# Kernel optimization log

Measured on AMD Instinct MI355X. Metric: run time of the kernel, lower is better.

Reference implementation:

```python
import jax, jax.numpy as jnp
import numpy as np

N_BINS = 15  # matches ECELoss(n_bins=15)


def setup_inputs() -> dict:
    key = jax.random.key(0)
    k1, k2 = jax.random.split(key)
    B, C = 2_097_152, 16
    logits = jax.random.normal(k1, (B, C), dtype=jnp.float32) * 2.0
    # binary multi-label targets, stored as float (forward casts to float anyway)
    targets = (jax.random.uniform(k2, (B, C)) < 0.5).astype(jnp.float32)
    return {"logits": logits, "targets": targets}


def reference(logits, targets):
    """Vectorized ECE: single bucketize + segment-sum pass replacing the
    per-class/per-bin Python loops. Same math: for each non-empty (class, bin)
    cell, accumulate |mean_conf - mean_acc| * (cell_count / B), then divide by
    the number of non-empty cells."""
    B, C = logits.shape
    probs = jax.nn.sigmoid(logits)  # [B, C]
    boundaries = jnp.linspace(0.0, 1.0, N_BINS + 1)
    # bin b satisfies boundaries[b] <= p < boundaries[b+1]  (>= start, < end)
    bin_idx = jnp.searchsorted(boundaries, probs, side="right") - 1  # [B, C]
    valid = (bin_idx >= 0) & (bin_idx < N_BINS)  # p == 1.0 falls in no bin
    seg = jnp.where(valid, jnp.arange(C)[None, :] * N_BINS + bin_idx, C * N_BINS)
    seg = seg.reshape(-1)
    num_seg = C * N_BINS + 1  # last segment = dumping ground for invalid
    ones = jnp.ones((B * C,), dtype=probs.dtype)
    cnt = jax.ops.segment_sum(ones, seg, num_segments=num_seg)[:-1]           # [C*n_bins]
    sum_p = jax.ops.segment_sum(probs.reshape(-1), seg, num_segments=num_seg)[:-1]
    sum_t = jax.ops.segment_sum(targets.reshape(-1), seg, num_segments=num_seg)[:-1]
    nonempty = cnt > 0
    safe = jnp.where(nonempty, cnt, 1.0)
    # |avg_confidence - accuracy| * mask.mean()  per non-empty cell
    term = jnp.abs(sum_p / safe - sum_t / safe) * (cnt / B)
    total = jnp.sum(jnp.where(nonempty, term, 0.0))
    count = jnp.sum(nonempty)
    return jnp.where(count > 0, total / count, jnp.zeros((), probs.dtype))
```

## Files before the change

### kernel.cpp

```cpp
#include <hip/hip_runtime.h>
#include <math.h>

#define NC 16
#define NBINS 15
#define NCELL (NC * NBINS)
#define GRID 2048
#define VITERS 16
#define BROWS 2097152.0
#define MAXREP 8

typedef float floatx4 __attribute__((ext_vector_type(4)));

template <int CTRL>
__device__ __forceinline__ unsigned int dpp_add(unsigned int v) {
    return v + (unsigned int)__builtin_amdgcn_update_dpp(0, (int)v, CTRL, 0xF, 0xF, true);
}

__device__ __forceinline__ float4 ldnt(const float4* p) {
    floatx4 v = __builtin_nontemporal_load((const floatx4*)p);
    return make_float4(v.x, v.y, v.z, v.w);
}

__global__ void __launch_bounds__(256, 4)
ece_partial(const float4* __restrict__ logits,
            const float4* __restrict__ targets,
            float* __restrict__ ws, int nrep) {
    __shared__ unsigned int h[64 * 60];

    const float LOG2E = 1.4426950408889634f;
    const int tid = blockIdx.x * 256 + threadIdx.x;
    const int S   = GRID * 256;

    unsigned int acc[4][NBINS];
#pragma unroll
    for (int j = 0; j < 4; ++j)
#pragma unroll
        for (int b = 0; b < NBINS; ++b) acc[j][b] = 0u;

    for (int k = 0; k < VITERS; k += 2) {
        int i0 = tid + k * S, i1 = i0 + S;
        float4 la[2], ta[2];
        la[0] = ldnt(&logits[i0]);
        la[1] = ldnt(&logits[i1]);
        ta[0] = targets[i0];
        ta[1] = targets[i1];
#pragma unroll
        for (int m = 0; m < 2; ++m) {
            float xs[4]  = {la[m].x, la[m].y, la[m].z, la[m].w};
            float tvs[4] = {ta[m].x, ta[m].y, ta[m].z, ta[m].w};
            int bs[4];
            unsigned int us[4];
#pragma unroll
            for (int j = 0; j < 4; ++j) {
                float e = __builtin_amdgcn_exp2f(-xs[j] * LOG2E);
                float p = __builtin_amdgcn_rcpf(1.0f + e);
                bs[j] = (int)(p * 15.0f);
                us[j] = (unsigned int)(fmaf(tvs[j], 262144.0f,
                                            fmaf(p, 1024.0f, 0.5f))) + (1u << 25);
            }
#pragma unroll
            for (int j = 0; j < 4; ++j)
#pragma unroll
                for (int b = 0; b < NBINS; ++b)
                    acc[j][b] += (bs[j] == b) ? us[j] : 0u;
        }
    }

#pragma unroll
    for (int j = 0; j < 4; ++j)
#pragma unroll
        for (int b = 0; b < NBINS; ++b) {
            unsigned int v = acc[j][b];
            v = dpp_add<0x114>(v);
            v = dpp_add<0x118>(v);
            acc[j][b] = v;
        }

    const int lane = threadIdx.x & 63;
    const int w    = threadIdx.x >> 6;
    const int r    = lane >> 4;
    const int q    = lane & 3;
    if ((lane & 15) >= 12) {
        unsigned int* dst = &h[((w * 4 + r) * 4 + q) * 60];
#pragma unroll
        for (int j = 0; j < 4; ++j)
#pragma unroll
            for (int b = 0; b < NBINS; ++b) dst[j * NBINS + b] = acc[j][b];
    }
    __syncthreads();

    const int t = threadIdx.x;
    if (t < NCELL) {
        const int bb = t >> 4;
        const int c  = t & 15;
        const int qq = c >> 2, jj = c & 3;
        unsigned int cnt = 0, tsum = 0, psum = 0;
#pragma unroll
        for (int m = 0; m < 16; ++m) {
            unsigned int v = h[(m * 4 + qq) * 60 + jj * NBINS + bb];
            cnt  += v >> 25;
            tsum += (v >> 18) & 127u;
            psum += v & 0x3FFFFu;
        }
        float* rp = ws + (blockIdx.x & (nrep - 1)) * (3 * NCELL);
        atomicAdd(&rp[t],             (float)cnt);
        atomicAdd(&rp[NCELL + t],     (float)psum * (1.0f / 1024.0f));
        atomicAdd(&rp[2 * NCELL + t], (float)tsum);
    }
}

__global__ void __launch_bounds__(256) ece_final(const float* __restrict__ ws,
                                                 float* __restrict__ out, int nrep) {
    __shared__ double s_term[256];
    __shared__ int s_ne[256];
    int i = threadIdx.x;
    double term = 0.0;
    int ne = 0;
    if (i < NCELL) {
        float cnt = 0.0f, sp = 0.0f, st = 0.0f;
        for (int rep = 0; rep < nrep; ++rep) {
            const float* r = ws + rep * (3 * NCELL);
            cnt += r[i];
            sp  += r[NCELL + i];
            st  += r[2 * NCELL + i];
        }
        if (cnt > 0.0f) {
            ne = 1;
            term = fabs((double)sp / (double)cnt - (double)st / (double)cnt) *
                   ((double)cnt / BROWS);
        }
    }
    s_term[i] = term;
    s_ne[i] = ne;
    __syncthreads();
    for (int off = 128; off > 0; off >>= 1) {
        if (i < off) {
            s_term[i] += s_term[i + off];
            s_ne[i]   += s_ne[i + off];
        }
        __syncthreads();
    }
    if (i == 0) out[0] = (s_ne[0] > 0) ? (float)(s_term[0] / (double)s_ne[0]) : 0.0f;
}

extern "C" void kernel_launch(void* const* d_in, const int* in_sizes, int n_in,
                              void* d_out, int out_size, void* d_ws, size_t ws_size,
                              hipStream_t stream) {
    const float4* logits  = (const float4*)d_in[0];
    const float4* targets = (const float4*)d_in[1];
    float* ws  = (float*)d_ws;
    float* out = (float*)d_out;

    int nrep = MAXREP;
    while (nrep > 1 && (size_t)(nrep * 3 * NCELL * sizeof(float)) > ws_size) nrep >>= 1;

    (void)hipMemsetAsync(ws, 0, nrep * 3 * NCELL * sizeof(float), stream);
    ece_partial<<<GRID, 256, 0, stream>>>(logits, targets, ws, nrep);
    ece_final<<<1, 256, 0, stream>>>(ws, out, nrep);
}
```

Baseline: 269.1 us.

## Replace register select-accumulate histogram with per-thread LDS atomic bins

Each thread now adds its packed value into a private column of a 64x256 LDS histogram with an atomic add, instead of running 15 compare-and-select adds per element in registers. Loads are batched four at a time instead of two. The aim is to cut the ALU work of the one-hot accumulation. The cost is 64 KB of LDS per block, which lowers occupancy (launch bounds go from 4 to 2), plus LDS atomic latency and extra barriers.

Result: no change. 270.3 us (+0.4%).

```diff
diff --git a/kernel.cpp b/kernel.cpp
--- a/kernel.cpp
+++ b/kernel.cpp
@@ -21,50 +21,53 @@
     return make_float4(v.x, v.y, v.z, v.w);
 }
 
-__global__ void __launch_bounds__(256, 4)
+__global__ void __launch_bounds__(256, 2)
 ece_partial(const float4* __restrict__ logits,
             const float4* __restrict__ targets,
             float* __restrict__ ws, int nrep) {
-    __shared__ unsigned int h[64 * 60];
+    __shared__ unsigned int h1[64 * 256];
 
     const float LOG2E = 1.4426950408889634f;
     const int tid = blockIdx.x * 256 + threadIdx.x;
     const int S   = GRID * 256;
+    const int col = threadIdx.x;
 
-    unsigned int acc[4][NBINS];
 #pragma unroll
-    for (int j = 0; j < 4; ++j)
+    for (int r = 0; r < 64; ++r) h1[r * 256 + col] = 0u;
+    __syncthreads();
+
+    for (int k = 0; k < VITERS; k += 4) {
+        float4 lv[4], tv[4];
 #pragma unroll
-        for (int b = 0; b < NBINS; ++b) acc[j][b] = 0u;
-
-    for (int k = 0; k < VITERS; k += 2) {
-        int i0 = tid + k * S, i1 = i0 + S;
-        float4 la[2], ta[2];
-        la[0] = ldnt(&logits[i0]);
-        la[1] = ldnt(&logits[i1]);
-        ta[0] = targets[i0];
-        ta[1] = targets[i1];
+        for (int m = 0; m < 4; ++m) {
+            int i = tid + (k + m) * S;
+            lv[m] = ldnt(&logits[i]);
+            tv[m] = targets[i];
+        }
 #pragma unroll
-        for (int m = 0; m < 2; ++m) {
-            float xs[4]  = {la[m].x, la[m].y, la[m].z, la[m].w};
-            float tvs[4] = {ta[m].x, ta[m].y, ta[m].z, ta[m].w};
-            int bs[4];
-            unsigned int us[4];
+        for (int m = 0; m < 4; ++m) {
+            float xs[4]  = {lv[m].x, lv[m].y, lv[m].z, lv[m].w};
+            float tvs[4] = {tv[m].x, tv[m].y, tv[m].z, tv[m].w};
 #pragma unroll
             for (int j = 0; j < 4; ++j) {
                 float e = __builtin_amdgcn_exp2f(-xs[j] * LOG2E);
                 float p = __builtin_amdgcn_rcpf(1.0f + e);
-                bs[j] = (int)(p * 15.0f);
-                us[j] = (unsigned int)(fmaf(tvs[j], 262144.0f,
-                                            fmaf(p, 1024.0f, 0.5f))) + (1u << 25);
+                int b = ((int)(p * 15.0f)) & 15;
+                unsigned int u = (unsigned int)(fmaf(tvs[j], 262144.0f,
+                                                     fmaf(p, 1024.0f, 0.5f))) +
+                                 (1u << 25);
+                atomicAdd(&h1[(b * 4 + j) * 256 + col], u);
             }
-#pragma unroll
-            for (int j = 0; j < 4; ++j)
-#pragma unroll
-                for (int b = 0; b < NBINS; ++b)
-                    acc[j][b] += (bs[j] == b) ? us[j] : 0u;
         }
     }
+    __syncthreads();
+
+    unsigned int acc[4][NBINS];
+#pragma unroll
+    for (int b = 0; b < NBINS; ++b)
+#pragma unroll
+        for (int j = 0; j < 4; ++j) acc[j][b] = h1[(b * 4 + j) * 256 + col];
+    __syncthreads();
 
 #pragma unroll
     for (int j = 0; j < 4; ++j)
@@ -81,7 +84,7 @@
     const int r    = lane >> 4;
     const int q    = lane & 3;
     if ((lane & 15) >= 12) {
-        unsigned int* dst = &h[((w * 4 + r) * 4 + q) * 60];
+        unsigned int* dst = &h1[((w * 4 + r) * 4 + q) * 60];
 #pragma unroll
         for (int j = 0; j < 4; ++j)
 #pragma unroll
@@ -97,7 +100,7 @@
         unsigned int cnt = 0, tsum = 0, psum = 0;
 #pragma unroll
         for (int m = 0; m < 16; ++m) {
-            unsigned int v = h[(m * 4 + qq) * 60 + jj * NBINS + bb];
+            unsigned int v = h1[(m * 4 + qq) * 60 + jj * NBINS + bb];
             cnt  += v >> 25;
             tsum += (v >> 18) & 127u;
             psum += v & 0x3FFFFu;
```
